# Performance work log

Hardware: AMD Instinct MI355X
Metric: run time of the kernel (lower is better)

## Reference

```python
import jax, jax.numpy as jnp
import numpy as np

B, S, E, H = 2, 2048, 1024, 16
DH = E // H  # 64


def setup_inputs() -> dict:
    key = jax.random.key(0)
    ks = jax.random.split(key, 9)
    sc = 1.0 / np.sqrt(E)
    return {
        "x": jax.random.normal(ks[0], (B, S, E), dtype=jnp.float32),
        "Wq": jax.random.normal(ks[1], (E, E), dtype=jnp.float32) * sc,
        "bq": jax.random.normal(ks[2], (E,), dtype=jnp.float32) * 0.02,
        "Wk": jax.random.normal(ks[3], (E, E), dtype=jnp.float32) * sc,
        "bk": jax.random.normal(ks[4], (E,), dtype=jnp.float32) * 0.02,
        "Wv": jax.random.normal(ks[5], (E, E), dtype=jnp.float32) * sc,
        "bv": jax.random.normal(ks[6], (E,), dtype=jnp.float32) * 0.02,
        "Wo": jax.random.normal(ks[7], (E, E), dtype=jnp.float32) * sc,
        "bo": jax.random.normal(ks[8], (E,), dtype=jnp.float32) * 0.02,
    }


def reference(x, Wq, bq, Wk, bk, Wv, bv, Wo, bo):
    b, s, e = x.shape
    h, dh = H, e // H
    # NOTE: original torch code does .view(B, H, S, Dh) on the [B, S, E]
    # projection WITHOUT transposing first; we replicate that exact reshape.
    q = (x @ Wq.T + bq).reshape(b, h, s, dh)
    k = (x @ Wk.T + bk).reshape(b, h, s, dh)
    v = (x @ Wv.T + bv).reshape(b, h, s, dh)
    scale = 1.0 / jnp.sqrt(jnp.asarray(dh, dtype=x.dtype))
    scores = jax.nn.softmax(jnp.einsum("bhqd,bhkd->bhqk", q, k) * scale, axis=-1)
    out = jnp.einsum("bhqk,bhkd->bhqd", scores, v)  # [B,H,S,Dh]
    out = out.transpose(0, 2, 1, 3).reshape(b, s, e)  # matches torch transpose(1,2).view
    return out @ Wo.T + bo
```

## Files before the change

### kernel.cpp

```cpp
#include <hip/hip_runtime.h>
#include <hip/hip_bf16.h>
#include <stdint.h>

typedef __bf16 bf16x8 __attribute__((ext_vector_type(8)));
typedef float  f32x4  __attribute__((ext_vector_type(4)));
typedef float  f32x16 __attribute__((ext_vector_type(16)));
typedef __hip_bfloat16 bf16;

__device__ __forceinline__ void gll16(const void* g, void* l) {
    typedef const unsigned int __attribute__((address_space(1)))* gp_t;
    typedef unsigned int __attribute__((address_space(3)))* lp_t;
    __builtin_amdgcn_global_load_lds((gp_t)(g), (lp_t)(l), 16, 0, 0);
}

__device__ __forceinline__ float fexp2(float x) {
#if __has_builtin(__builtin_amdgcn_exp2f)
    return __builtin_amdgcn_exp2f(x);
#else
    float r; asm volatile("v_exp_f32 %0, %1" : "=v"(r) : "v"(x)); return r;
#endif
}

__device__ __forceinline__ float tmax16(const f32x16& v) {
    float a0 = fmaxf(v[0], v[1]),   a1 = fmaxf(v[2], v[3]);
    float a2 = fmaxf(v[4], v[5]),   a3 = fmaxf(v[6], v[7]);
    float a4 = fmaxf(v[8], v[9]),   a5 = fmaxf(v[10], v[11]);
    float a6 = fmaxf(v[12], v[13]), a7 = fmaxf(v[14], v[15]);
    float b0 = fmaxf(a0, a1), b1 = fmaxf(a2, a3);
    float b2 = fmaxf(a4, a5), b3 = fmaxf(a6, a7);
    return fmaxf(fmaxf(b0, b1), fmaxf(b2, b3));
}
__device__ __forceinline__ float tsum16(const f32x16& v) {
    float a0 = v[0] + v[1],   a1 = v[2] + v[3];
    float a2 = v[4] + v[5],   a3 = v[6] + v[7];
    float a4 = v[8] + v[9],   a5 = v[10] + v[11];
    float a6 = v[12] + v[13], a7 = v[14] + v[15];
    float b0 = a0 + a1, b1 = a2 + a3, b2 = a4 + a5, b3 = a6 + a7;
    return (b0 + b1) + (b2 + b3);
}

__global__ __launch_bounds__(256) void prep_convert(
    const float* __restrict__ x,
    const float* __restrict__ wq, const float* __restrict__ wk,
    const float* __restrict__ wv, const float* __restrict__ wo,
    bf16* __restrict__ Xb, bf16* __restrict__ Wcat, bf16* __restrict__ Wob)
{
    int i = blockIdx.x * blockDim.x + threadIdx.x;
    int base = i * 4;
    const float* src; bf16* dst;
    if      (base < 4194304) { src = x  + base;             dst = Xb   + base; }
    else if (base < 5242880) { src = wq + (base - 4194304); dst = Wcat + (base - 4194304); }
    else if (base < 6291456) { src = wk + (base - 5242880); dst = Wcat + 1048576 + (base - 5242880); }
    else if (base < 7340032) { src = wv + (base - 6291456); dst = Wcat + 2097152 + (base - 6291456); }
    else                     { src = wo + (base - 7340032); dst = Wob  + (base - 7340032); }
    float4 v = *(const float4*)src;
    union { bf16 h[4]; ushort4 u; } cv;
    cv.h[0] = __float2bfloat16(v.x);
    cv.h[1] = __float2bfloat16(v.y);
    cv.h[2] = __float2bfloat16(v.z);
    cv.h[3] = __float2bfloat16(v.w);
    *(ushort4*)dst = cv.u;
}

__global__ __launch_bounds__(256, 2) void gemm_qkv(
    const bf16* __restrict__ X, const bf16* __restrict__ Wc,
    const float* __restrict__ bq, const float* __restrict__ bk, const float* __restrict__ bv,
    bf16* __restrict__ Pq, bf16* __restrict__ Pk, bf16* __restrict__ Pv)
{
    __shared__ __align__(16) bf16 Ab[128 * 32];
    __shared__ __align__(16) bf16 Bb[128 * 32];
    const int id = blockIdx.x;
    const int sid = (id & 7) * 96 + (id >> 3);
    const int t = threadIdx.x;
    const int lane = t & 63, w = t >> 6;
    const int lr = lane & 15, lg = lane >> 4;
    const int wr = w >> 1, wc = w & 1;
    const int row0 = (sid / 24) * 128, col0 = (sid % 24) * 128;

    f32x4 acc[4][4] = {};

    const char* Xc  = (const char*)X;
    const char* Wcc = (const char*)Wc;
    char* AbC = (char*)Ab;
    char* BbC = (char*)Bb;
    const int o0 = t * 16, o1 = o0 + 4096;
    const int ldsoff = w * 1024;

    for (int k0 = 0; k0 < 1024; k0 += 32) {
        __syncthreads();
        gll16(Xc  + (size_t)(row0 + (o0 >> 6)) * 2048 + (size_t)k0 * 2 + (o0 & 63), AbC + ldsoff);
        gll16(Wcc + (size_t)(col0 + (o0 >> 6)) * 2048 + (size_t)k0 * 2 + (o0 & 63), BbC + ldsoff);
        gll16(Xc  + (size_t)(row0 + (o1 >> 6)) * 2048 + (size_t)k0 * 2 + (o1 & 63), AbC + 4096 + ldsoff);
        gll16(Wcc + (size_t)(col0 + (o1 >> 6)) * 2048 + (size_t)k0 * 2 + (o1 & 63), BbC + 4096 + ldsoff);
        __syncthreads();
        bf16x8 af[4], bw[4];
        #pragma unroll
        for (int i = 0; i < 4; ++i)
            af[i] = *(const bf16x8*)(AbC + ((wr * 64 + i * 16 + lr) * 32 + lg * 8) * 2);
        #pragma unroll
        for (int j = 0; j < 4; ++j)
            bw[j] = *(const bf16x8*)(BbC + ((wc * 64 + j * 16 + lr) * 32 + lg * 8) * 2);
        #pragma unroll
        for (int i = 0; i < 4; ++i)
            #pragma unroll
            for (int j = 0; j < 4; ++j)
                acc[i][j] = __builtin_amdgcn_mfma_f32_16x16x32_bf16(af[i], bw[j], acc[i][j], 0, 0, 0);
    }

    const int mid = col0 >> 10;
    const float* bias = (mid == 0) ? bq : (mid == 1 ? bk : bv);
    bf16* Out = (mid == 0) ? Pq : (mid == 1 ? Pk : Pv);
    const float scale = (mid == 0) ? 0.125f * 1.44269504f : 1.0f;
    const int nc0 = col0 - (mid << 10) + wc * 64;
    const int mr0 = row0 + wr * 64;
    #pragma unroll
    for (int i = 0; i < 4; ++i)
        #pragma unroll
        for (int j = 0; j < 4; ++j) {
            int cc = nc0 + j * 16 + lr;
            float bsv = bias[cc];
            #pragma unroll
            for (int p = 0; p < 4; ++p) {
                int rr = mr0 + i * 16 + lg * 4 + p;
                Out[(size_t)rr * 1024 + cc] = __float2bfloat16((acc[i][j][p] + bsv) * scale);
            }
        }
}

__global__ __launch_bounds__(256) void transpose_v(const bf16* __restrict__ Pv, bf16* __restrict__ Vt)
{
    __shared__ bf16 tile[64][72];
    const int head = blockIdx.y;
    const int st   = blockIdx.x;
    const bf16* src = Pv + (size_t)head * 131072 + (size_t)st * 4096;
    bf16* dst = Vt + (size_t)head * 131072 + (size_t)st * 64;
    const int t = threadIdx.x;
    const int rr = t >> 2, c0 = (t & 3) * 16;
    #pragma unroll
    for (int u = 0; u < 2; ++u) {
        bf16x8 v = *(const bf16x8*)(src + rr * 64 + c0 + u * 8);
        #pragma unroll
        for (int e = 0; e < 8; ++e) tile[rr][c0 + u * 8 + e] = ((const bf16*)&v)[e];
    }
    __syncthreads();
    #pragma unroll
    for (int u = 0; u < 2; ++u) {
        bf16 ov[8];
        #pragma unroll
        for (int e = 0; e < 8; ++e) {
            int y = u * 8 + e;
            int z = (y & 3) | ((y & 8) >> 1) | ((y & 4) << 1);
            ov[e] = tile[c0 + z][rr];
        }
        *(bf16x8*)(dst + (size_t)rr * 2048 + c0 + u * 8) = *(const bf16x8*)ov;
    }
}

__global__ __launch_bounds__(256, 2) void attn_fwd(
    const bf16* __restrict__ Pq, const bf16* __restrict__ Pk,
    const bf16* __restrict__ Vt, bf16* __restrict__ Of)
{
    __shared__ __align__(16) bf16 Kl[2][128 * 64];
    __shared__ __align__(16) bf16 Vl[2][64 * 128];

    const int blk0 = blockIdx.x;
    const int blk = (blk0 & 7) * 64 + (blk0 >> 3);
    const int head = blk >> 4;
    const int qt = blk & 15;
    const int bb = head >> 4, hh = head & 15;
    const bf16* Qh = Pq + (size_t)head * 131072;
    const char* Khc = (const char*)(Pk + (size_t)head * 131072);
    const char* Vhc = (const char*)(Vt + (size_t)head * 131072);

    const int t = threadIdx.x;
    const int lane = t & 63, w = t >> 6;
    const int ql = lane & 31, hi = lane >> 5;
    const int q0 = qt * 128 + w * 32;

    bf16x8 qf[4];
    #pragma unroll
    for (int m = 0; m < 4; ++m)
        qf[m] = *(const bf16x8*)(Qh + (size_t)(q0 + ql) * 64 + m * 16 + hi * 8);

    f32x16 acc[2] = {};
    float m_run = -1e30f, l_run = 0.f;

    const int stg_o   = t * 16;
    const int stg_key = stg_o >> 7, stg_ks = (stg_o >> 4) & 7;
    const int stg_d   = stg_o >> 8, stg_vs = (stg_o >> 4) & 15;
    const size_t kgo = (size_t)stg_key * 128 + ((stg_ks ^ (stg_key & 7)) * 16);
    const size_t vgo = (size_t)stg_d * 4096 + ((stg_vs ^ (stg_d & 7)) * 16);
    const int ldst = w * 1024;

#define STAGE(S0, BUF)                                                          \
    {                                                                           \
        char* KB = (char*)(Kl[BUF]);                                            \
        char* VB = (char*)(Vl[BUF]);                                            \
        _Pragma("unroll")                                                       \
        for (int qq = 0; qq < 4; ++qq) {                                        \
            gll16(Khc + (size_t)(S0) * 128 + (size_t)qq * 4096 + kgo,           \
                  KB + qq * 4096 + ldst);                                       \
            gll16(Vhc + (size_t)(S0) * 2 + (size_t)qq * 65536 + vgo,            \
                  VB + qq * 4096 + ldst);                                       \
        }                                                                       \
    }

    STAGE(0, 0);
    STAGE(128, 1);

    int cur = 0;
    for (int s0 = 0; s0 < 2048; s0 += 128) {
        if (s0 < 1920) {
            asm volatile("s_waitcnt vmcnt(8)\n\ts_barrier" ::: "memory");
        } else {
            asm volatile("s_waitcnt vmcnt(0)\n\ts_barrier" ::: "memory");
        }

        const char* KlC = (const char*)(Kl[cur]);
        const char* VlC = (const char*)(Vl[cur]);

        f32x16 sa[4] = {};
        __builtin_amdgcn_s_setprio(1);
        #pragma unroll
        for (int kb = 0; kb < 4; ++kb) {
            int row = kb * 32 + ql;
            #pragma unroll
            for (int m = 0; m < 4; ++m) {
                int byt = row * 128 + ((32 * m + 16 * hi) ^ ((row & 7) << 4));
                bf16x8 kf = *(const bf16x8*)(KlC + byt);
                sa[kb] = __builtin_amdgcn_mfma_f32_32x32x16_bf16(kf, qf[m], sa[kb], 0, 0, 0);
            }
        }
        __builtin_amdgcn_s_setprio(0);

        float mx = fmaxf(fmaxf(tmax16(sa[0]), tmax16(sa[1])),
                         fmaxf(tmax16(sa[2]), tmax16(sa[3])));
        mx = fmaxf(mx, __shfl_xor(mx, 32));

        float mn;
        if (__all(mx - m_run <= 8.0f)) {
            mn = m_run;
        } else {
            mn = fmaxf(m_run, mx);
            float al = fexp2(m_run - mn);
            m_run = mn;
            l_run *= al;
            #pragma unroll
            for (int r = 0; r < 16; ++r) { acc[0][r] *= al; acc[1][r] *= al; }
        }

        #pragma unroll
        for (int kb = 0; kb < 4; ++kb)
            #pragma unroll
            for (int r = 0; r < 16; ++r)
                sa[kb][r] = fexp2(sa[kb][r] - mn);
        float rs = (tsum16(sa[0]) + tsum16(sa[1])) + (tsum16(sa[2]) + tsum16(sa[3]));
        rs += __shfl_xor(rs, 32);
        l_run += rs;

        __builtin_amdgcn_s_setprio(1);
        #pragma unroll
        for (int sb = 0; sb < 8; ++sb) {
            const int kb = sb >> 1, par = (sb & 1) * 8;
            bf16x8 pa;
            #pragma unroll
            for (int e = 0; e < 8; ++e) pa[e] = (__bf16)sa[kb][par + e];
            #pragma unroll
            for (int db = 0; db < 2; ++db) {
                int row = db * 32 + ql;
                int byt = row * 256 + ((sb * 32 + hi * 16) ^ ((row & 7) << 4));
                bf16x8 vf = *(const bf16x8*)(VlC + byt);
                acc[db] = __builtin_amdgcn_mfma_f32_32x32x16_bf16(vf, pa, acc[db], 0, 0, 0);
            }
        }
        __builtin_amdgcn_s_setprio(0);

        __builtin_amdgcn_s_barrier();
        if (s0 + 256 < 2048) STAGE(s0 + 256, cur);
        cur ^= 1;
    }
#undef STAGE

    float inv = 1.0f / l_run;
    bf16* orow = Of + (size_t)(bb * 2048 + q0 + ql) * 1024 + hh * 64;
    #pragma unroll
    for (int db = 0; db < 2; ++db)
        #pragma unroll
        for (int g = 0; g < 4; ++g) {
            union { bf16 h[4]; ushort4 u; } ob;
            #pragma unroll
            for (int j = 0; j < 4; ++j)
                ob.h[j] = __float2bfloat16(acc[db][4 * g + j] * inv);
            *(ushort4*)(orow + db * 32 + 8 * g + 4 * hi) = ob.u;
        }
}

__global__ __launch_bounds__(256, 2) void gemm_out(
    const bf16* __restrict__ A, const bf16* __restrict__ W,
    const float* __restrict__ bo, float* __restrict__ C)
{
    __shared__ __align__(16) bf16 Ab[128 * 32];
    __shared__ __align__(16) bf16 Bb[128 * 32];
    const int id = blockIdx.x;
    const int sid = (id & 7) * 32 + (id >> 3);
    const int t = threadIdx.x;
    const int lane = t & 63, w = t >> 6;
    const int lr = lane & 15, lg = lane >> 4;
    const int wr = w >> 1, wc = w & 1;
    const int row0 = (sid / 8) * 128, col0 = (sid % 8) * 128;

    f32x4 acc[4][4] = {};
    const char* Ac = (const char*)A;
    const char* Wc = (const char*)W;
    char* AbC = (char*)Ab;
    char* BbC = (char*)Bb;
    const int o0 = t * 16, o1 = o0 + 4096;
    const int ldsoff = w * 1024;

    for (int k0 = 0; k0 < 1024; k0 += 32) {
        __syncthreads();
        gll16(Ac + (size_t)(row0 + (o0 >> 6)) * 2048 + (size_t)k0 * 2 + (o0 & 63), AbC + ldsoff);
        gll16(Wc + (size_t)(col0 + (o0 >> 6)) * 2048 + (size_t)k0 * 2 + (o0 & 63), BbC + ldsoff);
        gll16(Ac + (size_t)(row0 + (o1 >> 6)) * 2048 + (size_t)k0 * 2 + (o1 & 63), AbC + 4096 + ldsoff);
        gll16(Wc + (size_t)(col0 + (o1 >> 6)) * 2048 + (size_t)k0 * 2 + (o1 & 63), BbC + 4096 + ldsoff);
        __syncthreads();
        bf16x8 af[4], bw[4];
        #pragma unroll
        for (int i = 0; i < 4; ++i)
            af[i] = *(const bf16x8*)(AbC + ((wr * 64 + i * 16 + lr) * 32 + lg * 8) * 2);
        #pragma unroll
        for (int j = 0; j < 4; ++j)
            bw[j] = *(const bf16x8*)(BbC + ((wc * 64 + j * 16 + lr) * 32 + lg * 8) * 2);
        #pragma unroll
        for (int i = 0; i < 4; ++i)
            #pragma unroll
            for (int j = 0; j < 4; ++j)
                acc[i][j] = __builtin_amdgcn_mfma_f32_16x16x32_bf16(af[i], bw[j], acc[i][j], 0, 0, 0);
    }

    const int nc0 = col0 + wc * 64;
    const int mr0 = row0 + wr * 64;
    #pragma unroll
    for (int i = 0; i < 4; ++i)
        #pragma unroll
        for (int j = 0; j < 4; ++j) {
            int cc = nc0 + j * 16 + lr;
            float bsv = bo[cc];
            #pragma unroll
            for (int p = 0; p < 4; ++p) {
                int rr = mr0 + i * 16 + lg * 4 + p;
                C[(size_t)rr * 1024 + cc] = acc[i][j][p] + bsv;
            }
        }
}

extern "C" void kernel_launch(void* const* d_in, const int* in_sizes, int n_in,
                              void* d_out, int out_size, void* d_ws, size_t ws_size,
                              hipStream_t stream) {
    const float* x  = (const float*)d_in[0];
    const float* Wq = (const float*)d_in[1];
    const float* bq = (const float*)d_in[2];
    const float* Wk = (const float*)d_in[3];
    const float* bk = (const float*)d_in[4];
    const float* Wv = (const float*)d_in[5];
    const float* bv = (const float*)d_in[6];
    const float* Wo = (const float*)d_in[7];
    const float* bo = (const float*)d_in[8];
    float* out = (float*)d_out;

    char* ws = (char*)d_ws;
    bf16* Xb   = (bf16*)(ws + 0);
    bf16* Wcat = (bf16*)(ws + 8388608);
    bf16* Wob  = (bf16*)(ws + 14680064);
    bf16* Pq   = (bf16*)(ws + 16777216);
    bf16* Pk   = (bf16*)(ws + 25165824);
    bf16* Pv   = (bf16*)(ws + 33554432);
    bf16* Vt   = (bf16*)(ws + 0);
    bf16* Of   = (bf16*)(ws + 33554432);
    (void)ws_size; (void)in_sizes; (void)n_in; (void)out_size;

    prep_convert<<<8192, 256, 0, stream>>>(x, Wq, Wk, Wv, Wo, Xb, Wcat, Wob);
    gemm_qkv<<<768, 256, 0, stream>>>(Xb, Wcat, bq, bk, bv, Pq, Pk, Pv);
    transpose_v<<<dim3(32, 32), 256, 0, stream>>>(Pv, Vt);
    attn_fwd<<<512, 256, 0, stream>>>(Pq, Pk, Vt, Of);
    gemm_out<<<256, 256, 0, stream>>>(Of, Wob, bo, out);
}
```

Measured before the change: 122.7 us.

## Split attention key tiles across two wave groups with LDS merge

Measured after the change: 122.9 us. About the same (+0.2%).

```diff
diff --git a/kernel.cpp b/kernel.cpp
--- a/kernel.cpp
+++ b/kernel.cpp
@@ -156,7 +156,7 @@
     }
 }
 
-__global__ __launch_bounds__(256, 2) void attn_fwd(
+__global__ __launch_bounds__(512, 4) void attn_fwd(
     const bf16* __restrict__ Pq, const bf16* __restrict__ Pk,
     const bf16* __restrict__ Vt, bf16* __restrict__ Of)
 {
@@ -174,8 +174,9 @@
 
     const int t = threadIdx.x;
     const int lane = t & 63, w = t >> 6;
+    const int qg = w & 3, kh = w >> 2;
     const int ql = lane & 31, hi = lane >> 5;
-    const int q0 = qt * 128 + w * 32;
+    const int q0 = qt * 128 + qg * 32;
 
     bf16x8 qf[4];
     #pragma unroll
@@ -185,9 +186,8 @@
     f32x16 acc[2] = {};
     float m_run = -1e30f, l_run = 0.f;
 
-    const int stg_o   = t * 16;
-    const int stg_key = stg_o >> 7, stg_ks = (stg_o >> 4) & 7;
-    const int stg_d   = stg_o >> 8, stg_vs = (stg_o >> 4) & 15;
+    const int stg_key = t >> 3, stg_ks = t & 7;
+    const int stg_d   = t >> 4, stg_vs = t & 15;
     const size_t kgo = (size_t)stg_key * 128 + ((stg_ks ^ (stg_key & 7)) * 16);
     const size_t vgo = (size_t)stg_d * 4096 + ((stg_vs ^ (stg_d & 7)) * 16);
     const int ldst = w * 1024;
@@ -197,11 +197,11 @@
         char* KB = (char*)(Kl[BUF]);                                            \
         char* VB = (char*)(Vl[BUF]);                                            \
         _Pragma("unroll")                                                       \
-        for (int qq = 0; qq < 4; ++qq) {                                        \
-            gll16(Khc + (size_t)(S0) * 128 + (size_t)qq * 4096 + kgo,           \
-                  KB + qq * 4096 + ldst);                                       \
-            gll16(Vhc + (size_t)(S0) * 2 + (size_t)qq * 65536 + vgo,            \
-                  VB + qq * 4096 + ldst);                                       \
+        for (int qq = 0; qq < 2; ++qq) {                                        \
+            gll16(Khc + (size_t)(S0) * 128 + (size_t)qq * 8192 + kgo,           \
+                  KB + qq * 8192 + ldst);                                       \
+            gll16(Vhc + (size_t)(S0) * 2 + (size_t)qq * 131072 + vgo,           \
+                  VB + qq * 8192 + ldst);                                       \
         }                                                                       \
     }
 
@@ -211,7 +211,7 @@
     int cur = 0;
     for (int s0 = 0; s0 < 2048; s0 += 128) {
         if (s0 < 1920) {
-            asm volatile("s_waitcnt vmcnt(8)\n\ts_barrier" ::: "memory");
+            asm volatile("s_waitcnt vmcnt(4)\n\ts_barrier" ::: "memory");
         } else {
             asm volatile("s_waitcnt vmcnt(0)\n\ts_barrier" ::: "memory");
         }
@@ -219,11 +219,11 @@
         const char* KlC = (const char*)(Kl[cur]);
         const char* VlC = (const char*)(Vl[cur]);
 
-        f32x16 sa[4] = {};
+        f32x16 sa[2] = {};
         __builtin_amdgcn_s_setprio(1);
         #pragma unroll
-        for (int kb = 0; kb < 4; ++kb) {
-            int row = kb * 32 + ql;
+        for (int kb = 0; kb < 2; ++kb) {
+            int row = kh * 64 + kb * 32 + ql;
             #pragma unroll
             for (int m = 0; m < 4; ++m) {
                 int byt = row * 128 + ((32 * m + 16 * hi) ^ ((row & 7) << 4));
@@ -233,8 +233,7 @@
         }
         __builtin_amdgcn_s_setprio(0);
 
-        float mx = fmaxf(fmaxf(tmax16(sa[0]), tmax16(sa[1])),
-                         fmaxf(tmax16(sa[2]), tmax16(sa[3])));
+        float mx = fmaxf(tmax16(sa[0]), tmax16(sa[1]));
         mx = fmaxf(mx, __shfl_xor(mx, 32));
 
         float mn;
@@ -250,25 +249,26 @@
         }
 
         #pragma unroll
-        for (int kb = 0; kb < 4; ++kb)
+        for (int kb = 0; kb < 2; ++kb)
             #pragma unroll
             for (int r = 0; r < 16; ++r)
                 sa[kb][r] = fexp2(sa[kb][r] - mn);
-        float rs = (tsum16(sa[0]) + tsum16(sa[1])) + (tsum16(sa[2]) + tsum16(sa[3]));
+        float rs = tsum16(sa[0]) + tsum16(sa[1]);
         rs += __shfl_xor(rs, 32);
         l_run += rs;
 
         __builtin_amdgcn_s_setprio(1);
         #pragma unroll
-        for (int sb = 0; sb < 8; ++sb) {
-            const int kb = sb >> 1, par = (sb & 1) * 8;
+        for (int sbl = 0; sbl < 4; ++sbl) {
+            const int kb = sbl >> 1, par = (sbl & 1) * 8;
+            const int sbg = kh * 4 + sbl;
             bf16x8 pa;
             #pragma unroll
             for (int e = 0; e < 8; ++e) pa[e] = (__bf16)sa[kb][par + e];
             #pragma unroll
             for (int db = 0; db < 2; ++db) {
                 int row = db * 32 + ql;
-                int byt = row * 256 + ((sb * 32 + hi * 16) ^ ((row & 7) << 4));
+                int byt = row * 256 + ((sbg * 32 + hi * 16) ^ ((row & 7) << 4));
                 bf16x8 vf = *(const bf16x8*)(VlC + byt);
                 acc[db] = __builtin_amdgcn_mfma_f32_32x32x16_bf16(vf, pa, acc[db], 0, 0, 0);
             }
@@ -281,18 +281,38 @@
     }
 #undef STAGE
 
-    float inv = 1.0f / l_run;
-    bf16* orow = Of + (size_t)(bb * 2048 + q0 + ql) * 1024 + hh * 64;
-    #pragma unroll
-    for (int db = 0; db < 2; ++db)
-        #pragma unroll
-        for (int g = 0; g < 4; ++g) {
-            union { bf16 h[4]; ushort4 u; } ob;
-            #pragma unroll
-            for (int j = 0; j < 4; ++j)
-                ob.h[j] = __float2bfloat16(acc[db][4 * g + j] * inv);
-            *(ushort4*)(orow + db * 32 + 8 * g + 4 * hi) = ob.u;
-        }
+    float* cb1 = (float*)Kl;
+    float* cb2 = (float*)Vl;
+    const int idx = qg * 64 + lane;
+    if (kh == 1) {
+        #pragma unroll
+        for (int r = 0; r < 16; ++r) cb1[idx * 18 + r] = acc[0][r];
+        cb1[idx * 18 + 16] = m_run;
+        cb1[idx * 18 + 17] = l_run;
+        #pragma unroll
+        for (int r = 0; r < 16; ++r) cb2[idx * 17 + r] = acc[1][r];
+    }
+    __syncthreads();
+    if (kh == 0) {
+        float m1 = cb1[idx * 18 + 16], l1 = cb1[idx * 18 + 17];
+        float mN = fmaxf(m_run, m1);
+        float a0 = fexp2(m_run - mN), a1 = fexp2(m1 - mN);
+        float inv = 1.0f / (l_run * a0 + l1 * a1);
+        bf16* orow = Of + (size_t)(bb * 2048 + q0 + ql) * 1024 + hh * 64;
+        #pragma unroll
+        for (int db = 0; db < 2; ++db)
+            #pragma unroll
+            for (int g = 0; g < 4; ++g) {
+                union { bf16 h[4]; ushort4 u; } ob;
+                #pragma unroll
+                for (int j = 0; j < 4; ++j) {
+                    int r = 4 * g + j;
+                    float p1 = (db == 0) ? cb1[idx * 18 + r] : cb2[idx * 17 + r];
+                    ob.h[j] = __float2bfloat16((acc[db][r] * a0 + p1 * a1) * inv);
+                }
+                *(ushort4*)(orow + db * 32 + 8 * g + 4 * hi) = ob.u;
+            }
+    }
 }
 
 __global__ __launch_bounds__(256, 2) void gemm_out(
@@ -382,6 +402,6 @@
     prep_convert<<<8192, 256, 0, stream>>>(x, Wq, Wk, Wv, Wo, Xb, Wcat, Wob);
     gemm_qkv<<<768, 256, 0, stream>>>(Xb, Wcat, bq, bk, bv, Pq, Pk, Pv);
     transpose_v<<<dim3(32, 32), 256, 0, stream>>>(Pv, Vt);
-    attn_fwd<<<512, 256, 0, stream>>>(Pq, Pk, Vt, Of);
+    attn_fwd<<<512, 512, 0, stream>>>(Pq, Pk, Vt, Of);
     gemm_out<<<256, 256, 0, stream>>>(Of, Wob, bo, out);
 }
```
